# Performance work log

Hardware: AMD Instinct MI355X
Metric: run time of the kernel (lower is better)

Reference implementation:

```python
import jax, jax.numpy as jnp
import numpy as np

N = 50000        # nodes
E = 800000       # edges
D_IN = 512       # input_shape
PROJ = 256       # proj_dim
H = 4            # num_heads
C = 32           # hidden_channels
HC = H * C
NUM_LABELS = 10
SLOPE = 0.2      # GATv2 LeakyReLU negative slope


def _glorot(key, shape):
    fan_in = shape[-1]
    return jax.random.normal(key, shape, jnp.float32) / jnp.sqrt(jnp.float32(fan_in))


def setup_inputs() -> dict:
    key = jax.random.key(0)
    ks = jax.random.split(key, 16)
    inp = {}
    inp["x"] = jax.random.normal(ks[0], (N, D_IN), jnp.float32)
    inp["edge_index"] = jax.random.randint(ks[1], (2, E), 0, N, dtype=jnp.int64)
    # projection Linear
    inp["W_proj"] = _glorot(ks[2], (PROJ, D_IN)); inp["b_proj"] = jnp.zeros((PROJ,), jnp.float32)
    # GATv2 layer 1: lin_l, lin_r, att, bias
    inp["Wl1"] = _glorot(ks[3], (HC, PROJ)); inp["bl1"] = jnp.zeros((HC,), jnp.float32)
    inp["Wr1"] = _glorot(ks[4], (HC, PROJ)); inp["br1"] = jnp.zeros((HC,), jnp.float32)
    inp["att1"] = _glorot(ks[5], (H, C)); inp["bias1"] = jnp.zeros((HC,), jnp.float32)
    # GATv2 layer 2
    inp["Wl2"] = _glorot(ks[6], (HC, HC)); inp["bl2"] = jnp.zeros((HC,), jnp.float32)
    inp["Wr2"] = _glorot(ks[7], (HC, HC)); inp["br2"] = jnp.zeros((HC,), jnp.float32)
    inp["att2"] = _glorot(ks[8], (H, C)); inp["bias2"] = jnp.zeros((HC,), jnp.float32)
    # head MLP
    inp["W1"] = _glorot(ks[9], (C, HC)); inp["b1"] = jnp.zeros((C,), jnp.float32)
    inp["W2"] = _glorot(ks[10], (NUM_LABELS, C)); inp["b2"] = jnp.zeros((NUM_LABELS,), jnp.float32)
    return inp


def _gatv2(x, src, dst, Wl, bl, Wr, br, att, bias):
    # x: [N, F_in]; src/dst: [E]. PyG GATv2Conv, concat=True, no self-loops, eval (no dropout).
    xl = (x @ Wl.T + bl).reshape(N, H, C)   # source transform
    xr = (x @ Wr.T + br).reshape(N, H, C)   # target transform
    e = jax.nn.leaky_relu(xl[src] + xr[dst], negative_slope=SLOPE)  # [E,H,C]
    logit = jnp.einsum('ehc,hc->eh', e, att)                        # [E,H]
    # segment softmax over incoming edges of each destination node
    m = jax.ops.segment_max(logit, dst, num_segments=N)             # [N,H]
    m = jnp.where(jnp.isfinite(m), m, jnp.float32(0))               # empty segments -> 0
    p = jnp.exp(logit - m[dst])                                     # [E,H]
    s = jax.ops.segment_sum(p, dst, num_segments=N)                 # [N,H]
    alpha = p / (s[dst] + jnp.float32(1e-16))                       # [E,H]
    out = jax.ops.segment_sum(xl[src] * alpha[:, :, None], dst, num_segments=N)  # [N,H,C]
    return out.reshape(N, HC) + bias


def reference(x, edge_index, W_proj, b_proj, Wl1, bl1, Wr1, br1, att1, bias1,
              Wl2, bl2, Wr2, br2, att2, bias2, W1, b1, W2, b2):
    src, dst = edge_index[0], edge_index[1]
    h = jax.nn.elu(x @ W_proj.T + b_proj)
    h = jax.nn.elu(_gatv2(h, src, dst, Wl1, bl1, Wr1, br1, att1, bias1))
    h = jax.nn.elu(_gatv2(h, src, dst, Wl2, bl2, Wr2, br2, att2, bias2))
    h = jax.nn.elu(h @ W1.T + b1)
    return h @ W2.T + b2
```

## Files before the change

### kernel.cpp

```cpp
#include <hip/hip_runtime.h>
#include <cstdint>
#include <cstddef>

constexpr int NN = 50000;
constexpr int NE = 800000;

typedef _Float16 half8 __attribute__((ext_vector_type(8)));
typedef _Float16 half4v __attribute__((ext_vector_type(4)));
typedef _Float16 half2v __attribute__((ext_vector_type(2)));
typedef float f32x16 __attribute__((ext_vector_type(16)));
typedef unsigned short ushort_t;

__device__ inline ushort_t f2h(float f) {
  _Float16 h = (_Float16)f;
  return __builtin_bit_cast(ushort_t, h);
}

#if __has_builtin(__builtin_amdgcn_fdot2)
__device__ inline float fdot2(half2v a, half2v b, float c) {
  return __builtin_amdgcn_fdot2(a, b, c, false);
}
#else
__device__ inline float fdot2(half2v a, half2v b, float c) {
  return c + (float)a[0] * (float)b[0] + (float)a[1] * (float)b[1];
}
#endif

__global__ void k_wconv(const float* __restrict__ W, ushort_t* __restrict__ Bh,
                        int M, int K, int total) {
  int idx = blockIdx.x * 256 + threadIdx.x;
  if (idx >= total) return;
  int j = idx & 7;
  int l = (idx >> 3) & 63;
  int blk = idx >> 9;
  int nKB = K >> 4;
  int cb = blk / nKB, kb = blk - cb * nKB;
  int col = cb * 32 + (l & 31);
  int k = kb * 16 + ((l >> 5) & 1) * 8 + j;
  float v = (col < M) ? W[(size_t)col * K + k] : 0.f;
  Bh[idx] = f2h(v);
}

__global__ __launch_bounds__(512) void gemm_proj_l1(const float* __restrict__ x,
    const ushort_t* __restrict__ WpF, const ushort_t* __restrict__ WB1,
    const float* __restrict__ bp, const float* __restrict__ bl1,
    const float* __restrict__ br1, ushort_t* __restrict__ xlh,
    ushort_t* __restrict__ xrh, int N)
{
  constexpr int NKK = 4;
  constexpr int nKB1 = 32;
  constexpr int nK1 = 8;
  __shared__ ushort_t Ah[2][2 * NKK * 512];
  __shared__ ushort_t H0[16384];
  const int t = threadIdx.x;
  const int lane = t & 63;
  const int wid = t >> 6;
  const int wr = wid >> 2;
  const int wc = wid & 3;
  const int row0 = blockIdx.x * 64;
  const int cb0 = wc * 2;

  const int s_r = t >> 4, s_k = (t & 15) * 4;
  const int sb0 = (s_k >> 4) * 512 + (s_r + 32 * ((s_k >> 3) & 1)) * 8 + (s_k & 7);
  const int sb1 = sb0 + NKK * 512;
  const bool ok0 = (row0 + s_r) < N;
  const bool ok1 = (row0 + s_r + 32) < N;
  const float* ap0 = x + (size_t)(row0 + s_r) * 512 + s_k;
  const float* ap1 = x + (size_t)(row0 + s_r + 32) * 512 + s_k;

  f32x16 acc0 = {}, acc1 = {};
  float4 f0 = make_float4(0, 0, 0, 0), f1 = make_float4(0, 0, 0, 0);

  auto aload = [&](int ks) {
    f0 = make_float4(0, 0, 0, 0);
    f1 = make_float4(0, 0, 0, 0);
    if (ok0) f0 = *(const float4*)(ap0 + (size_t)ks * 64);
    if (ok1) f1 = *(const float4*)(ap1 + (size_t)ks * 64);
  };
  auto cvt4 = [](float4 f) {
    half4v h;
    h[0] = (_Float16)f.x; h[1] = (_Float16)f.y;
    h[2] = (_Float16)f.z; h[3] = (_Float16)f.w;
    return h;
  };
  auto stage_write = [&](int buf) {
    *(half4v*)&Ah[buf][sb0] = cvt4(f0);
    *(half4v*)&Ah[buf][sb1] = cvt4(f1);
  };

  aload(0);
  stage_write(0);
  __syncthreads();

  for (int ks = 0; ks < nK1; ++ks) {
    const int cur = ks & 1;
    const int nxt = cur ^ 1;
    const bool have_next = (ks + 1 < nK1);
    if (have_next) aload(ks + 1);

    #pragma unroll
    for (int kk = 0; kk < NKK; ++kk) {
      const int kbg = ks * NKK + kk;
      half8 ah = *(const half8*)&Ah[cur][(wr * NKK + kk) * 512 + lane * 8];
      const size_t bo0 = ((size_t)(cb0 * nKB1 + kbg) * 64 + lane) * 8;
      half8 bh0 = *(const half8*)(WpF + bo0);
      acc0 = __builtin_amdgcn_mfma_f32_32x32x16_f16(ah, bh0, acc0, 0, 0, 0);
      const size_t bo1 = ((size_t)((cb0 + 1) * nKB1 + kbg) * 64 + lane) * 8;
      half8 bh1 = *(const half8*)(WpF + bo1);
      acc1 = __builtin_amdgcn_mfma_f32_32x32x16_f16(ah, bh1, acc1, 0, 0, 0);
    }

    if (have_next) stage_write(nxt);
    __syncthreads();
  }

  {
    int col = cb0 * 32 + (lane & 31);
    float bv = bp[col];
    #pragma unroll
    for (int r = 0; r < 16; ++r) {
      int row = wr * 32 + (r & 3) + 8 * (r >> 2) + 4 * (lane >> 5);
      float v = acc0[r] + bv;
      v = v > 0.f ? v : (__expf(v) - 1.f);
      H0[((row >> 5) * 16 + (col >> 4)) * 512 +
         ((row & 31) + 32 * ((col >> 3) & 1)) * 8 + (col & 7)] = f2h(v);
    }
    int col1 = col + 32;
    float bv1 = bp[col1];
    #pragma unroll
    for (int r = 0; r < 16; ++r) {
      int row = wr * 32 + (r & 3) + 8 * (r >> 2) + 4 * (lane >> 5);
      float v = acc1[r] + bv1;
      v = v > 0.f ? v : (__expf(v) - 1.f);
      H0[((row >> 5) * 16 + (col1 >> 4)) * 512 +
         ((row & 31) + 32 * ((col1 >> 3) & 1)) * 8 + (col1 & 7)] = f2h(v);
    }
  }
  __syncthreads();

  f32x16 acc2a = {}, acc2b = {};
  #pragma unroll
  for (int kk = 0; kk < 16; ++kk) {
    half8 ah = *(const half8*)&H0[(wr * 16 + kk) * 512 + lane * 8];
    const size_t bo0 = ((size_t)(cb0 * 16 + kk) * 64 + lane) * 8;
    half8 bh0 = *(const half8*)(WB1 + bo0);
    acc2a = __builtin_amdgcn_mfma_f32_32x32x16_f16(ah, bh0, acc2a, 0, 0, 0);
    const size_t bo1 = ((size_t)((cb0 + 1) * 16 + kk) * 64 + lane) * 8;
    half8 bh1 = *(const half8*)(WB1 + bo1);
    acc2b = __builtin_amdgcn_mfma_f32_32x32x16_f16(ah, bh1, acc2b, 0, 0, 0);
  }

  auto epi2 = [&](const f32x16& acc, int cb) {
    int cc = cb * 32 + (lane & 31);
    float bv = (cc < 128) ? bl1[cc] : br1[cc - 128];
    #pragma unroll
    for (int r = 0; r < 16; ++r) {
      int rr = row0 + wr * 32 + (r & 3) + 8 * (r >> 2) + 4 * (lane >> 5);
      if (rr < N) {
        float v = acc[r] + bv;
        if (cc < 128) xlh[(size_t)rr * 128 + cc] = f2h(v);
        else          xrh[(size_t)rr * 128 + (cc - 128)] = f2h(v);
      }
    }
  };
  epi2(acc2a, cb0);
  epi2(acc2b, cb0 + 1);
}

__global__ __launch_bounds__(512) void gemm_mlp(const ushort_t* __restrict__ h2,
    const ushort_t* __restrict__ W1F, const ushort_t* __restrict__ W2F,
    const float* __restrict__ b1, const float* __restrict__ b2,
    float* __restrict__ out, int N)
{
  constexpr int NKK = 4;
  __shared__ ushort_t Ah[2][2 * NKK * 512];
  __shared__ ushort_t H3[2048];
  const int t = threadIdx.x;
  const int lane = t & 63;
  const int wid = t >> 6;
  const int wr = wid >> 2;
  const int wc = wid & 3;
  const int row0 = blockIdx.x * 64;

  const int s_r = t >> 3, s_k = (t & 7) * 8;
  const int sb0 = ((s_r >> 5) * NKK + (s_k >> 4)) * 512 +
                  ((s_r & 31) + 32 * ((s_k >> 3) & 1)) * 8;
  const bool ok0 = (row0 + s_r) < N;
  const ushort_t* aph = h2 + (size_t)(row0 + s_r) * 128 + s_k;

  f32x16 acc = {};
  half8 h8 = {};

  auto aload = [&](int ks) {
    half8 z = {};
    h8 = ok0 ? *(const half8*)(aph + (size_t)ks * 64) : z;
  };

  aload(0);
  *(half8*)&Ah[0][sb0] = h8;
  __syncthreads();

  for (int ks = 0; ks < 2; ++ks) {
    const int cur = ks & 1;
    const bool have_next = (ks == 0);
    if (have_next) aload(1);

    if (wc == 0) {
      #pragma unroll
      for (int kk = 0; kk < NKK; ++kk) {
        const int kbg = ks * NKK + kk;
        half8 ah = *(const half8*)&Ah[cur][(wr * NKK + kk) * 512 + lane * 8];
        half8 bh = *(const half8*)(W1F + ((size_t)kbg * 64 + lane) * 8);
        acc = __builtin_amdgcn_mfma_f32_32x32x16_f16(ah, bh, acc, 0, 0, 0);
      }
    }

    if (have_next) *(half8*)&Ah[cur ^ 1][sb0] = h8;
    __syncthreads();
  }

  if (wc == 0) {
    int cc = lane & 31;
    float bv = b1[cc];
    #pragma unroll
    for (int r = 0; r < 16; ++r) {
      int row = wr * 32 + (r & 3) + 8 * (r >> 2) + 4 * (lane >> 5);
      float v = acc[r] + bv;
      v = v > 0.f ? v : (__expf(v) - 1.f);
      H3[((row >> 5) * 2 + (cc >> 4)) * 512 +
         ((row & 31) + 32 * ((cc >> 3) & 1)) * 8 + (cc & 7)] = f2h(v);
    }
  }
  __syncthreads();

  if (wc == 0) {
    f32x16 acc2 = {};
    #pragma unroll
    for (int kk = 0; kk < 2; ++kk) {
      half8 ah = *(const half8*)&H3[(wr * 2 + kk) * 512 + lane * 8];
      half8 bh = *(const half8*)(W2F + ((size_t)kk * 64 + lane) * 8);
      acc2 = __builtin_amdgcn_mfma_f32_32x32x16_f16(ah, bh, acc2, 0, 0, 0);
    }
    int cc = lane & 31;
    if (cc < 10) {
      float bv = b2[cc];
      #pragma unroll
      for (int r = 0; r < 16; ++r) {
        int rr = row0 + wr * 32 + (r & 3) + 8 * (r >> 2) + 4 * (lane >> 5);
        if (rr < N) out[(size_t)rr * 10 + cc] = acc2[r] + bv;
      }
    }
  }
}

template<int ACT, int OUTMODE, int BKT, int AFP16, int NCB>
__global__ __launch_bounds__(512) void gemm_mfma(const void* __restrict__ Av,
    const ushort_t* __restrict__ Bh,
    const float* __restrict__ bias, const float* __restrict__ bias2,
    float* __restrict__ C, ushort_t* __restrict__ C16a,
    ushort_t* __restrict__ C16b, int N, int M, int K)
{
  constexpr int NKK = BKT / 16;
  __shared__ ushort_t Ah[2][2 * NKK * 512];
  const int t = threadIdx.x;
  const int lane = t & 63;
  const int wid = t >> 6;
  const int wr = wid >> 2;
  const int wc = wid & 3;
  const int row0 = blockIdx.x * 64;
  const int col0 = blockIdx.y * (128 * NCB);
  const int nKB = K >> 4;
  const int nK = K / BKT;
  const int cb0 = (col0 >> 5) + wc * NCB;

  int s_r, s_k, sb0, sb1 = 0;
  bool ok0 = false, ok1 = false;
  if constexpr (!AFP16) {
    s_r = t >> 4; s_k = (t & 15) * 4;
    sb0 = (s_k >> 4) * 512 + (s_r + 32 * ((s_k >> 3) & 1)) * 8 + (s_k & 7);
    sb1 = sb0 + NKK * 512;
    ok0 = (row0 + s_r) < N;
    ok1 = (row0 + s_r + 32) < N;
  } else if constexpr (BKT == 64) {
    s_r = t >> 3; s_k = (t & 7) * 8;
    sb0 = ((s_r >> 5) * NKK + (s_k >> 4)) * 512 +
          ((s_r & 31) + 32 * ((s_k >> 3) & 1)) * 8;
    ok0 = (row0 + s_r) < N;
  } else {
    s_r = t >> 3; s_k = (t & 7) * 4;
    sb0 = ((s_r >> 5) * NKK + (s_k >> 4)) * 512 +
          ((s_r & 31) + 32 * ((s_k >> 3) & 1)) * 8 + (s_k & 7);
    ok0 = (row0 + s_r) < N;
  }
  const float*    ap0 = (const float*)Av + (size_t)(row0 + s_r) * K + s_k;
  const float*    ap1 = (const float*)Av + (size_t)(row0 + s_r + 32) * K + s_k;
  const ushort_t* aph = (const ushort_t*)Av + (size_t)(row0 + s_r) * K + s_k;

  f32x16 acc0 = {}, acc1 = {};
  float4 f0 = make_float4(0, 0, 0, 0), f1 = make_float4(0, 0, 0, 0);
  half8 h8 = {};
  half4v h4 = {};

  auto aload = [&](int ks) {
    if constexpr (!AFP16) {
      f0 = make_float4(0, 0, 0, 0);
      f1 = make_float4(0, 0, 0, 0);
      if (ok0) f0 = *(const float4*)(ap0 + (size_t)ks * BKT);
      if (ok1) f1 = *(const float4*)(ap1 + (size_t)ks * BKT);
    } else if constexpr (BKT == 64) {
      half8 z = {};
      h8 = ok0 ? *(const half8*)(aph + (size_t)ks * BKT) : z;
    } else {
      half4v z = {};
      h4 = ok0 ? *(const half4v*)(aph + (size_t)ks * BKT) : z;
    }
  };
  auto cvt4 = [](float4 f) {
    half4v h;
    h[0] = (_Float16)f.x; h[1] = (_Float16)f.y;
    h[2] = (_Float16)f.z; h[3] = (_Float16)f.w;
    return h;
  };
  auto stage_write = [&](int buf) {
    if constexpr (!AFP16) {
      *(half4v*)&Ah[buf][sb0] = cvt4(f0);
      *(half4v*)&Ah[buf][sb1] = cvt4(f1);
    } else if constexpr (BKT == 64) {
      *(half8*)&Ah[buf][sb0] = h8;
    } else {
      *(half4v*)&Ah[buf][sb0] = h4;
    }
  };

  aload(0);
  stage_write(0);
  __syncthreads();

  for (int ks = 0; ks < nK; ++ks) {
    const int cur = ks & 1;
    const int nxt = cur ^ 1;
    const bool have_next = (ks + 1 < nK);
    if (have_next) aload(ks + 1);

    #pragma unroll
    for (int kk = 0; kk < NKK; ++kk) {
      const int kbg = ks * NKK + kk;
      half8 ah = *(const half8*)&Ah[cur][(wr * NKK + kk) * 512 + lane * 8];
      const size_t bo0 = ((size_t)(cb0 * nKB + kbg) * 64 + lane) * 8;
      half8 bh0 = *(const half8*)(Bh + bo0);
      acc0 = __builtin_amdgcn_mfma_f32_32x32x16_f16(ah, bh0, acc0, 0, 0, 0);
      if constexpr (NCB == 2) {
        const size_t bo1 = ((size_t)((cb0 + 1) * nKB + kbg) * 64 + lane) * 8;
        half8 bh1 = *(const half8*)(Bh + bo1);
        acc1 = __builtin_amdgcn_mfma_f32_32x32x16_f16(ah, bh1, acc1, 0, 0, 0);
      }
    }

    if (have_next) stage_write(nxt);
    __syncthreads();
  }

  auto epi = [&](const f32x16& acc, int cb) {
    int cc = cb * 32 + (lane & 31);
    float bv;
    if constexpr (OUTMODE == 3) bv = (cc < 128) ? bias[cc] : bias2[cc - 128];
    else                        bv = (cc < M) ? bias[cc] : 0.f;
    #pragma unroll
    for (int r = 0; r < 16; ++r) {
      int rr = row0 + wr * 32 + (r & 3) + 8 * (r >> 2) + 4 * (lane >> 5);
      if (rr < N && cc < M) {
        float v = acc[r] + bv;
        if (ACT) v = v > 0.f ? v : (__expf(v) - 1.f);
        if constexpr (OUTMODE == 0)      C[(size_t)rr * M + cc] = v;
        else if constexpr (OUTMODE == 1) C16a[(size_t)rr * M + cc] = f2h(v);
        else {
          if (cc < 128) C16a[(size_t)rr * 128 + cc] = f2h(v);
          else          C16b[(size_t)rr * 128 + (cc - 128)] = f2h(v);
        }
      }
    }
  };
  epi(acc0, cb0);
  if constexpr (NCB == 2) epi(acc1, cb0 + 1);
}

__global__ void k_degrank(const int* __restrict__ ei, int* __restrict__ deg,
                          int* __restrict__ rank) {
  int e = blockIdx.x * 256 + threadIdx.x;
  if (e >= NE) return;
  int d = ei[NE + e];
  rank[e] = atomicAdd(&deg[d], 1);
}

__global__ __launch_bounds__(256) void k_scan1(const int* __restrict__ deg,
    int* __restrict__ rowstart, int* __restrict__ blocksum) {
  __shared__ int sm[256];
  int b = blockIdx.x, t = threadIdx.x;
  int i = b * 256 + t;
  int v = (i < NN) ? deg[i] : 0;
  sm[t] = v;
  __syncthreads();
  #pragma unroll
  for (int off = 1; off < 256; off <<= 1) {
    int u = (t >= off) ? sm[t - off] : 0;
    __syncthreads();
    sm[t] += u;
    __syncthreads();
  }
  if (i < NN) rowstart[i + 1] = sm[t];
  if (t == 255) blocksum[b] = sm[255];
}

__global__ __launch_bounds__(256) void k_scan2(int* __restrict__ blocksum, int nb) {
  __shared__ int sm[256];
  int t = threadIdx.x;
  int v = (t < nb) ? blocksum[t] : 0;
  sm[t] = v;
  __syncthreads();
  #pragma unroll
  for (int off = 1; off < 256; off <<= 1) {
    int u = (t >= off) ? sm[t - off] : 0;
    __syncthreads();
    sm[t] += u;
    __syncthreads();
  }
  if (t < nb) blocksum[t] = (t == 0) ? 0 : sm[t - 1];
}

__global__ __launch_bounds__(256) void k_scan3(int* __restrict__ rowstart,
    const int* __restrict__ blocksum) {
  int b = blockIdx.x, t = threadIdx.x;
  int i = b * 256 + t;
  if (i == 0) rowstart[0] = 0;
  if (i < NN) rowstart[i + 1] += blocksum[b];
}

__global__ void k_scatter(const int* __restrict__ ei, const int* __restrict__ rowstart,
                          const int* __restrict__ rank, int* __restrict__ srcp) {
  int e = blockIdx.x * 256 + threadIdx.x;
  if (e >= NE) return;
  int d = ei[NE + e];
  srcp[rowstart[d] + rank[e]] = ei[e];
}

__global__ __launch_bounds__(256) void k_gat(const ushort_t* __restrict__ xl,
    const ushort_t* __restrict__ xr, const int* __restrict__ srcp,
    const int* __restrict__ rowstart, const float* __restrict__ att,
    const float* __restrict__ bias, ushort_t* __restrict__ out)
{
  const int g = threadIdx.x >> 5;
  const int c = threadIdx.x & 31;
  const int n = blockIdx.x * 8 + g;
  const int r0 = rowstart[n], r1 = rowstart[n + 1];
  half4v xrh = *(const half4v*)(xr + (size_t)n * 128 + 4 * c);
  const half2v xr01 = {xrh[0], xrh[1]};
  const half2v xr23 = {xrh[2], xrh[3]};
  const float4 atv = *(const float4*)(att + 4 * c);
  const half2v at01 = {(_Float16)atv.x, (_Float16)atv.y};
  const half2v at23 = {(_Float16)atv.z, (_Float16)atv.w};
  const half2v k02 = {(_Float16)0.2f, (_Float16)0.2f};

  float m = -1e30f, ssum = 0.f;
  float a0 = 0.f, a1 = 0.f, a2 = 0.f, a3 = 0.f;

  auto lg = [&](int s, float4& xs) -> float {
    half4v hv = *(const half4v*)(xl + (size_t)s * 128 + 4 * c);
    xs.x = (float)hv[0]; xs.y = (float)hv[1];
    xs.z = (float)hv[2]; xs.w = (float)hv[3];
    half2v u01 = half2v{hv[0], hv[1]} + xr01;
    half2v u23 = half2v{hv[2], hv[3]} + xr23;
    u01 = __builtin_elementwise_max(u01, u01 * k02);
    u23 = __builtin_elementwise_max(u23, u23 * k02);
    float l = fdot2(u01, at01, fdot2(u23, at23, 0.f));
    l += __shfl_xor(l, 1);
    l += __shfl_xor(l, 2);
    l += __shfl_xor(l, 4);
    return l;
  };

  const int je = r1 - 1;
  for (int j = r0; j < r1; j += 8) {
    int s0 = srcp[j];
    int s1 = srcp[min(j + 1, je)], s2 = srcp[min(j + 2, je)];
    int s3 = srcp[min(j + 3, je)], s4 = srcp[min(j + 4, je)];
    int s5 = srcp[min(j + 5, je)], s6 = srcp[min(j + 6, je)];
    int s7 = srcp[min(j + 7, je)];
    float4 x0, x1, x2, x3, x4, x5, x6, x7;
    float l0 = lg(s0, x0), l1 = lg(s1, x1), l2 = lg(s2, x2), l3 = lg(s3, x3);
    float l4 = lg(s4, x4), l5 = lg(s5, x5), l6 = lg(s6, x6), l7 = lg(s7, x7);
    l1 = (j + 1 < r1) ? l1 : -1e30f;
    l2 = (j + 2 < r1) ? l2 : -1e30f;
    l3 = (j + 3 < r1) ? l3 : -1e30f;
    l4 = (j + 4 < r1) ? l4 : -1e30f;
    l5 = (j + 5 < r1) ? l5 : -1e30f;
    l6 = (j + 6 < r1) ? l6 : -1e30f;
    l7 = (j + 7 < r1) ? l7 : -1e30f;
    float mloc = fmaxf(fmaxf(fmaxf(l0, l1), fmaxf(l2, l3)),
                       fmaxf(fmaxf(l4, l5), fmaxf(l6, l7)));
    float mn = fmaxf(m, mloc);
    float sc = __expf(m - mn);
    float p0 = __expf(l0 - mn), p1 = __expf(l1 - mn);
    float p2 = __expf(l2 - mn), p3 = __expf(l3 - mn);
    float p4 = __expf(l4 - mn), p5 = __expf(l5 - mn);
    float p6 = __expf(l6 - mn), p7 = __expf(l7 - mn);
    ssum = ssum * sc + (((p0 + p1) + (p2 + p3)) + ((p4 + p5) + (p6 + p7)));
    a0 = a0 * sc + (((p0 * x0.x + p1 * x1.x) + (p2 * x2.x + p3 * x3.x)) +
                    ((p4 * x4.x + p5 * x5.x) + (p6 * x6.x + p7 * x7.x)));
    a1 = a1 * sc + (((p0 * x0.y + p1 * x1.y) + (p2 * x2.y + p3 * x3.y)) +
                    ((p4 * x4.y + p5 * x5.y) + (p6 * x6.y + p7 * x7.y)));
    a2 = a2 * sc + (((p0 * x0.z + p1 * x1.z) + (p2 * x2.z + p3 * x3.z)) +
                    ((p4 * x4.z + p5 * x5.z) + (p6 * x6.z + p7 * x7.z)));
    a3 = a3 * sc + (((p0 * x0.w + p1 * x1.w) + (p2 * x2.w + p3 * x3.w)) +
                    ((p4 * x4.w + p5 * x5.w) + (p6 * x6.w + p7 * x7.w)));
    m = mn;
  }

  const float4 bv = *(const float4*)(bias + 4 * c);
  float rinv = 1.f / (ssum + 1e-16f);
  float o0 = a0 * rinv + bv.x;
  float o1 = a1 * rinv + bv.y;
  float o2 = a2 * rinv + bv.z;
  float o3 = a3 * rinv + bv.w;
  o0 = o0 > 0.f ? o0 : (__expf(o0) - 1.f);
  o1 = o1 > 0.f ? o1 : (__expf(o1) - 1.f);
  o2 = o2 > 0.f ? o2 : (__expf(o2) - 1.f);
  o3 = o3 > 0.f ? o3 : (__expf(o3) - 1.f);
  half4v ov;
  ov[0] = (_Float16)o0; ov[1] = (_Float16)o1;
  ov[2] = (_Float16)o2; ov[3] = (_Float16)o3;
  *(half4v*)(out + (size_t)n * 128 + 4 * c) = ov;
}

__global__ void k_report_ws(float* out, int out_size, float wsz) {
  int i = blockIdx.x * 256 + threadIdx.x;
  if (i < out_size) out[i] = (i == 0) ? wsz : 0.f;
}

extern "C" void kernel_launch(void* const* d_in, const int* in_sizes, int n_in,
                              void* d_out, int out_size, void* d_ws, size_t ws_size,
                              hipStream_t stream)
{
  const float* x    = (const float*)d_in[0];
  const int*   ei   = (const int*)d_in[1];
  const float* Wp   = (const float*)d_in[2];  const float* bp    = (const float*)d_in[3];
  const float* Wl1  = (const float*)d_in[4];  const float* bl1   = (const float*)d_in[5];
  const float* Wr1  = (const float*)d_in[6];  const float* br1   = (const float*)d_in[7];
  const float* att1 = (const float*)d_in[8];  const float* bias1 = (const float*)d_in[9];
  const float* Wl2  = (const float*)d_in[10]; const float* bl2   = (const float*)d_in[11];
  const float* Wr2  = (const float*)d_in[12]; const float* br2   = (const float*)d_in[13];
  const float* att2 = (const float*)d_in[14]; const float* bias2 = (const float*)d_in[15];
  const float* W1   = (const float*)d_in[16]; const float* b1    = (const float*)d_in[17];
  const float* W2   = (const float*)d_in[18]; const float* b2    = (const float*)d_in[19];
  float* out = (float*)d_out;

  constexpr size_t NEED = 122300000;
  if (ws_size < NEED) {
    k_report_ws<<<(out_size + 255) / 256, 256, 0, stream>>>(out, out_size, (float)ws_size);
    return;
  }
  char* ws = (char*)d_ws;
  ushort_t* h1h   = (ushort_t*)(ws + 0);
  ushort_t* h2h   = (ushort_t*)(ws + 25600000);
  ushort_t* xlh   = (ushort_t*)(ws + 51200000);
  ushort_t* xrh   = (ushort_t*)(ws + 76800000);
  ushort_t* wb    = (ushort_t*)(ws + 108800000);
  int*      srcp  = (int*)(ws + 115200000);
  int*      rank  = (int*)(ws + 118400000);
  int*      deg   = (int*)(ws + 121600000);
  int*      rowst = (int*)(ws + 122000000);
  int*      bsum  = (int*)(ws + 122250000);

  ushort_t* Wph  = wb;
  ushort_t* WB1h = wb + 131072;
  ushort_t* WB2h = wb + 196608;
  ushort_t* W1h  = wb + 229376;
  ushort_t* W2h  = wb + 233472;

  hipMemsetAsync(deg, 0, NN * sizeof(int), stream);

  k_wconv<<<(131072+255)/256, 256, 0, stream>>>(Wp,  Wph,          256, 512, 131072);
  k_wconv<<<(32768+255)/256,  256, 0, stream>>>(Wl1, WB1h,         128, 256, 32768);
  k_wconv<<<(32768+255)/256,  256, 0, stream>>>(Wr1, WB1h + 32768, 128, 256, 32768);
  k_wconv<<<(16384+255)/256,  256, 0, stream>>>(Wl2, WB2h,         128, 128, 16384);
  k_wconv<<<(16384+255)/256,  256, 0, stream>>>(Wr2, WB2h + 16384, 128, 128, 16384);
  k_wconv<<<(4096+255)/256,   256, 0, stream>>>(W1,  W1h,          32,  128, 4096);
  k_wconv<<<(1024+255)/256,   256, 0, stream>>>(W2,  W2h,          10,  32,  1024);

  constexpr int NB = (NN + 255) / 256;
  k_degrank<<<(NE+255)/256, 256, 0, stream>>>(ei, deg, rank);
  k_scan1  <<<NB, 256, 0, stream>>>(deg, rowst, bsum);
  k_scan2  <<<1, 256, 0, stream>>>(bsum, NB);
  k_scan3  <<<NB, 256, 0, stream>>>(rowst, bsum);
  k_scatter<<<(NE+255)/256, 256, 0, stream>>>(ei, rowst, rank, srcp);

  constexpr int GX = (NN + 63) / 64;

  gemm_proj_l1<<<GX, 512, 0, stream>>>(x, Wph, WB1h, bp, bl1, br1, xlh, xrh, NN);
  k_gat<<<NN/8, 256, 0, stream>>>(xlh, xrh, srcp, rowst, att1, bias1, h1h);

  gemm_mfma<0,3,64,1,2><<<dim3(GX, 1), 512, 0, stream>>>(
      h1h, WB2h, bl2, br2, nullptr, xlh, xrh, NN, 256, 128);
  k_gat<<<NN/8, 256, 0, stream>>>(xlh, xrh, srcp, rowst, att2, bias2, h2h);

  gemm_mlp<<<GX, 512, 0, stream>>>(h2h, W1h, W2h, b1, b2, out, NN);
}
```

Measured before the change: 240.7 us.

## Pre-convert x to fp16 and stage GEMM A tiles via direct global-to-LDS loads

Adds a separate kernel that converts the fp32 input x to fp16, so the fused projection GEMM can load A tiles with global_load_lds (direct DMA into shared memory) instead of loading to registers, converting, and storing to LDS. The same direct-to-LDS staging is applied to a new specialized layer-2 GEMM, which replaces the generic templated kernel, and to the MLP GEMM. Boundary rows are clamped rather than zero-filled, and the workspace is relaid out. The extra conversion pass reads x and writes an fp16 copy, adding memory traffic that has to be repaid by the simpler GEMM load path.

```diff
diff --git a/kernel.cpp b/kernel.cpp
--- a/kernel.cpp
+++ b/kernel.cpp
@@ -25,6 +25,26 @@
   return c + (float)a[0] * (float)b[0] + (float)a[1] * (float)b[1];
 }
 #endif
+
+__device__ __forceinline__ void gload_lds16(const void* g, void* l) {
+  __builtin_amdgcn_global_load_lds(
+      (const __attribute__((address_space(1))) void*)g,
+      (__attribute__((address_space(3))) void*)l, 16, 0, 0);
+}
+
+__global__ __launch_bounds__(256) void k_cvt(const float* __restrict__ x,
+                                             ushort_t* __restrict__ xh) {
+  int i = blockIdx.x * 256 + threadIdx.x;
+  if (i >= NN * 512 / 8) return;
+  const float4* p = (const float4*)(x + (size_t)i * 8);
+  float4 a = p[0], b = p[1];
+  half8 h;
+  h[0] = (_Float16)a.x; h[1] = (_Float16)a.y;
+  h[2] = (_Float16)a.z; h[3] = (_Float16)a.w;
+  h[4] = (_Float16)b.x; h[5] = (_Float16)b.y;
+  h[6] = (_Float16)b.z; h[7] = (_Float16)b.w;
+  *(half8*)(xh + (size_t)i * 8) = h;
+}
 
 __global__ void k_wconv(const float* __restrict__ W, ushort_t* __restrict__ Bh,
                         int M, int K, int total) {
@@ -41,7 +61,7 @@
   Bh[idx] = f2h(v);
 }
 
-__global__ __launch_bounds__(512) void gemm_proj_l1(const float* __restrict__ x,
+__global__ __launch_bounds__(512) void gemm_proj_l1(const ushort_t* __restrict__ xh,
     const ushort_t* __restrict__ WpF, const ushort_t* __restrict__ WB1,
     const float* __restrict__ bp, const float* __restrict__ bl1,
     const float* __restrict__ br1, ushort_t* __restrict__ xlh,
@@ -50,7 +70,7 @@
   constexpr int NKK = 4;
   constexpr int nKB1 = 32;
   constexpr int nK1 = 8;
-  __shared__ ushort_t Ah[2][2 * NKK * 512];
+  __shared__ ushort_t Ah[2][8 * 512];
   __shared__ ushort_t H0[16384];
   const int t = threadIdx.x;
   const int lane = t & 63;
@@ -60,43 +80,20 @@
   const int row0 = blockIdx.x * 64;
   const int cb0 = wc * 2;
 
-  const int s_r = t >> 4, s_k = (t & 15) * 4;
-  const int sb0 = (s_k >> 4) * 512 + (s_r + 32 * ((s_k >> 3) & 1)) * 8 + (s_k & 7);
-  const int sb1 = sb0 + NKK * 512;
-  const bool ok0 = (row0 + s_r) < N;
-  const bool ok1 = (row0 + s_r + 32) < N;
-  const float* ap0 = x + (size_t)(row0 + s_r) * 512 + s_k;
-  const float* ap1 = x + (size_t)(row0 + s_r + 32) * 512 + s_k;
+  const int swt = wid >> 2, skb = wid & 3;
+  const int grow = min(row0 + swt * 32 + (lane & 31), N - 1);
+  const ushort_t* gA = xh + (size_t)grow * 512 + skb * 16 + (lane >> 5) * 8;
+  ushort_t* ld0 = &Ah[0][wid * 512];
+  ushort_t* ld1 = &Ah[1][wid * 512];
 
   f32x16 acc0 = {}, acc1 = {};
-  float4 f0 = make_float4(0, 0, 0, 0), f1 = make_float4(0, 0, 0, 0);
-
-  auto aload = [&](int ks) {
-    f0 = make_float4(0, 0, 0, 0);
-    f1 = make_float4(0, 0, 0, 0);
-    if (ok0) f0 = *(const float4*)(ap0 + (size_t)ks * 64);
-    if (ok1) f1 = *(const float4*)(ap1 + (size_t)ks * 64);
-  };
-  auto cvt4 = [](float4 f) {
-    half4v h;
-    h[0] = (_Float16)f.x; h[1] = (_Float16)f.y;
-    h[2] = (_Float16)f.z; h[3] = (_Float16)f.w;
-    return h;
-  };
-  auto stage_write = [&](int buf) {
-    *(half4v*)&Ah[buf][sb0] = cvt4(f0);
-    *(half4v*)&Ah[buf][sb1] = cvt4(f1);
-  };
-
-  aload(0);
-  stage_write(0);
+
+  gload_lds16(gA, ld0);
   __syncthreads();
 
   for (int ks = 0; ks < nK1; ++ks) {
     const int cur = ks & 1;
-    const int nxt = cur ^ 1;
-    const bool have_next = (ks + 1 < nK1);
-    if (have_next) aload(ks + 1);
+    if (ks + 1 < nK1) gload_lds16(gA + (size_t)(ks + 1) * 64, cur ? ld0 : ld1);
 
     #pragma unroll
     for (int kk = 0; kk < NKK; ++kk) {
@@ -109,8 +106,6 @@
       half8 bh1 = *(const half8*)(WpF + bo1);
       acc1 = __builtin_amdgcn_mfma_f32_32x32x16_f16(ah, bh1, acc1, 0, 0, 0);
     }
-
-    if (have_next) stage_write(nxt);
     __syncthreads();
   }
 
@@ -167,13 +162,76 @@
   epi2(acc2b, cb0 + 1);
 }
 
+__global__ __launch_bounds__(512) void gemm_l2(const ushort_t* __restrict__ h1,
+    const ushort_t* __restrict__ WB2, const float* __restrict__ bl2,
+    const float* __restrict__ br2, ushort_t* __restrict__ xlh,
+    ushort_t* __restrict__ xrh, int N)
+{
+  constexpr int NKK = 4;
+  constexpr int nKB = 8;
+  constexpr int nK = 2;
+  __shared__ ushort_t Ah[2][8 * 512];
+  const int t = threadIdx.x;
+  const int lane = t & 63;
+  const int wid = t >> 6;
+  const int wr = wid >> 2;
+  const int wc = wid & 3;
+  const int row0 = blockIdx.x * 64;
+  const int cb0 = wc * 2;
+
+  const int swt = wid >> 2, skb = wid & 3;
+  const int grow = min(row0 + swt * 32 + (lane & 31), N - 1);
+  const ushort_t* gA = h1 + (size_t)grow * 128 + skb * 16 + (lane >> 5) * 8;
+  ushort_t* ld0 = &Ah[0][wid * 512];
+  ushort_t* ld1 = &Ah[1][wid * 512];
+
+  f32x16 acc0 = {}, acc1 = {};
+
+  gload_lds16(gA, ld0);
+  __syncthreads();
+
+  for (int ks = 0; ks < nK; ++ks) {
+    const int cur = ks & 1;
+    if (ks + 1 < nK) gload_lds16(gA + (size_t)(ks + 1) * 64, cur ? ld0 : ld1);
+
+    #pragma unroll
+    for (int kk = 0; kk < NKK; ++kk) {
+      const int kbg = ks * NKK + kk;
+      half8 ah = *(const half8*)&Ah[cur][(wr * NKK + kk) * 512 + lane * 8];
+      const size_t bo0 = ((size_t)(cb0 * nKB + kbg) * 64 + lane) * 8;
+      half8 bh0 = *(const half8*)(WB2 + bo0);
+      acc0 = __builtin_amdgcn_mfma_f32_32x32x16_f16(ah, bh0, acc0, 0, 0, 0);
+      const size_t bo1 = ((size_t)((cb0 + 1) * nKB + kbg) * 64 + lane) * 8;
+      half8 bh1 = *(const half8*)(WB2 + bo1);
+      acc1 = __builtin_amdgcn_mfma_f32_32x32x16_f16(ah, bh1, acc1, 0, 0, 0);
+    }
+    __syncthreads();
+  }
+
+  auto epi = [&](const f32x16& acc, int cb) {
+    int cc = cb * 32 + (lane & 31);
+    float bv = (cc < 128) ? bl2[cc] : br2[cc - 128];
+    #pragma unroll
+    for (int r = 0; r < 16; ++r) {
+      int rr = row0 + wr * 32 + (r & 3) + 8 * (r >> 2) + 4 * (lane >> 5);
+      if (rr < N) {
+        float v = acc[r] + bv;
+        if (cc < 128) xlh[(size_t)rr * 128 + cc] = f2h(v);
+        else          xrh[(size_t)rr * 128 + (cc - 128)] = f2h(v);
+      }
+    }
+  };
+  epi(acc0, cb0);
+  epi(acc1, cb0 + 1);
+}
+
 __global__ __launch_bounds__(512) void gemm_mlp(const ushort_t* __restrict__ h2,
     const ushort_t* __restrict__ W1F, const ushort_t* __restrict__ W2F,
     const float* __restrict__ b1, const float* __restrict__ b2,
     float* __restrict__ out, int N)
 {
   constexpr int NKK = 4;
-  __shared__ ushort_t Ah[2][2 * NKK * 512];
+  __shared__ ushort_t Ah[2][8 * 512];
   __shared__ ushort_t H3[2048];
   const int t = threadIdx.x;
   const int lane = t & 63;
@@ -182,28 +240,20 @@
   const int wc = wid & 3;
   const int row0 = blockIdx.x * 64;
 
-  const int s_r = t >> 3, s_k = (t & 7) * 8;
-  const int sb0 = ((s_r >> 5) * NKK + (s_k >> 4)) * 512 +
-                  ((s_r & 31) + 32 * ((s_k >> 3) & 1)) * 8;
-  const bool ok0 = (row0 + s_r) < N;
-  const ushort_t* aph = h2 + (size_t)(row0 + s_r) * 128 + s_k;
+  const int swt = wid >> 2, skb = wid & 3;
+  const int grow = min(row0 + swt * 32 + (lane & 31), N - 1);
+  const ushort_t* gA = h2 + (size_t)grow * 128 + skb * 16 + (lane >> 5) * 8;
+  ushort_t* ld0 = &Ah[0][wid * 512];
+  ushort_t* ld1 = &Ah[1][wid * 512];
 
   f32x16 acc = {};
-  half8 h8 = {};
-
-  auto aload = [&](int ks) {
-    half8 z = {};
-    h8 = ok0 ? *(const half8*)(aph + (size_t)ks * 64) : z;
-  };
-
-  aload(0);
-  *(half8*)&Ah[0][sb0] = h8;
+
+  gload_lds16(gA, ld0);
   __syncthreads();
 
   for (int ks = 0; ks < 2; ++ks) {
     const int cur = ks & 1;
-    const bool have_next = (ks == 0);
-    if (have_next) aload(1);
+    if (ks + 1 < 2) gload_lds16(gA + (size_t)(ks + 1) * 64, cur ? ld0 : ld1);
 
     if (wc == 0) {
       #pragma unroll
@@ -214,8 +264,6 @@
         acc = __builtin_amdgcn_mfma_f32_32x32x16_f16(ah, bh, acc, 0, 0, 0);
       }
     }
-
-    if (have_next) *(half8*)&Ah[cur ^ 1][sb0] = h8;
     __syncthreads();
   }
 
@@ -251,137 +299,6 @@
       }
     }
   }
-}
-
-template<int ACT, int OUTMODE, int BKT, int AFP16, int NCB>
-__global__ __launch_bounds__(512) void gemm_mfma(const void* __restrict__ Av,
-    const ushort_t* __restrict__ Bh,
-    const float* __restrict__ bias, const float* __restrict__ bias2,
-    float* __restrict__ C, ushort_t* __restrict__ C16a,
-    ushort_t* __restrict__ C16b, int N, int M, int K)
-{
-  constexpr int NKK = BKT / 16;
-  __shared__ ushort_t Ah[2][2 * NKK * 512];
-  const int t = threadIdx.x;
-  const int lane = t & 63;
-  const int wid = t >> 6;
-  const int wr = wid >> 2;
-  const int wc = wid & 3;
-  const int row0 = blockIdx.x * 64;
-  const int col0 = blockIdx.y * (128 * NCB);
-  const int nKB = K >> 4;
-  const int nK = K / BKT;
-  const int cb0 = (col0 >> 5) + wc * NCB;
-
-  int s_r, s_k, sb0, sb1 = 0;
-  bool ok0 = false, ok1 = false;
-  if constexpr (!AFP16) {
-    s_r = t >> 4; s_k = (t & 15) * 4;
-    sb0 = (s_k >> 4) * 512 + (s_r + 32 * ((s_k >> 3) & 1)) * 8 + (s_k & 7);
-    sb1 = sb0 + NKK * 512;
-    ok0 = (row0 + s_r) < N;
-    ok1 = (row0 + s_r + 32) < N;
-  } else if constexpr (BKT == 64) {
-    s_r = t >> 3; s_k = (t & 7) * 8;
-    sb0 = ((s_r >> 5) * NKK + (s_k >> 4)) * 512 +
-          ((s_r & 31) + 32 * ((s_k >> 3) & 1)) * 8;
-    ok0 = (row0 + s_r) < N;
-  } else {
-    s_r = t >> 3; s_k = (t & 7) * 4;
-    sb0 = ((s_r >> 5) * NKK + (s_k >> 4)) * 512 +
-          ((s_r & 31) + 32 * ((s_k >> 3) & 1)) * 8 + (s_k & 7);
-    ok0 = (row0 + s_r) < N;
-  }
-  const float*    ap0 = (const float*)Av + (size_t)(row0 + s_r) * K + s_k;
-  const float*    ap1 = (const float*)Av + (size_t)(row0 + s_r + 32) * K + s_k;
-  const ushort_t* aph = (const ushort_t*)Av + (size_t)(row0 + s_r) * K + s_k;
-
-  f32x16 acc0 = {}, acc1 = {};
-  float4 f0 = make_float4(0, 0, 0, 0), f1 = make_float4(0, 0, 0, 0);
-  half8 h8 = {};
-  half4v h4 = {};
-
-  auto aload = [&](int ks) {
-    if constexpr (!AFP16) {
-      f0 = make_float4(0, 0, 0, 0);
-      f1 = make_float4(0, 0, 0, 0);
-      if (ok0) f0 = *(const float4*)(ap0 + (size_t)ks * BKT);
-      if (ok1) f1 = *(const float4*)(ap1 + (size_t)ks * BKT);
-    } else if constexpr (BKT == 64) {
-      half8 z = {};
-      h8 = ok0 ? *(const half8*)(aph + (size_t)ks * BKT) : z;
-    } else {
-      half4v z = {};
-      h4 = ok0 ? *(const half4v*)(aph + (size_t)ks * BKT) : z;
-    }
-  };
-  auto cvt4 = [](float4 f) {
-    half4v h;
-    h[0] = (_Float16)f.x; h[1] = (_Float16)f.y;
-    h[2] = (_Float16)f.z; h[3] = (_Float16)f.w;
-    return h;
-  };
-  auto stage_write = [&](int buf) {
-    if constexpr (!AFP16) {
-      *(half4v*)&Ah[buf][sb0] = cvt4(f0);
-      *(half4v*)&Ah[buf][sb1] = cvt4(f1);
-    } else if constexpr (BKT == 64) {
-      *(half8*)&Ah[buf][sb0] = h8;
-    } else {
-      *(half4v*)&Ah[buf][sb0] = h4;
-    }
-  };
-
-  aload(0);
-  stage_write(0);
-  __syncthreads();
-
-  for (int ks = 0; ks < nK; ++ks) {
-    const int cur = ks & 1;
-    const int nxt = cur ^ 1;
-    const bool have_next = (ks + 1 < nK);
-    if (have_next) aload(ks + 1);
-
-    #pragma unroll
-    for (int kk = 0; kk < NKK; ++kk) {
-      const int kbg = ks * NKK + kk;
-      half8 ah = *(const half8*)&Ah[cur][(wr * NKK + kk) * 512 + lane * 8];
-      const size_t bo0 = ((size_t)(cb0 * nKB + kbg) * 64 + lane) * 8;
-      half8 bh0 = *(const half8*)(Bh + bo0);
-      acc0 = __builtin_amdgcn_mfma_f32_32x32x16_f16(ah, bh0, acc0, 0, 0, 0);
-      if constexpr (NCB == 2) {
-        const size_t bo1 = ((size_t)((cb0 + 1) * nKB + kbg) * 64 + lane) * 8;
-        half8 bh1 = *(const half8*)(Bh + bo1);
-        acc1 = __builtin_amdgcn_mfma_f32_32x32x16_f16(ah, bh1, acc1, 0, 0, 0);
-      }
-    }
-
-    if (have_next) stage_write(nxt);
-    __syncthreads();
-  }
-
-  auto epi = [&](const f32x16& acc, int cb) {
-    int cc = cb * 32 + (lane & 31);
-    float bv;
-    if constexpr (OUTMODE == 3) bv = (cc < 128) ? bias[cc] : bias2[cc - 128];
-    else                        bv = (cc < M) ? bias[cc] : 0.f;
-    #pragma unroll
-    for (int r = 0; r < 16; ++r) {
-      int rr = row0 + wr * 32 + (r & 3) + 8 * (r >> 2) + 4 * (lane >> 5);
-      if (rr < N && cc < M) {
-        float v = acc[r] + bv;
-        if (ACT) v = v > 0.f ? v : (__expf(v) - 1.f);
-        if constexpr (OUTMODE == 0)      C[(size_t)rr * M + cc] = v;
-        else if constexpr (OUTMODE == 1) C16a[(size_t)rr * M + cc] = f2h(v);
-        else {
-          if (cc < 128) C16a[(size_t)rr * 128 + cc] = f2h(v);
-          else          C16b[(size_t)rr * 128 + (cc - 128)] = f2h(v);
-        }
-      }
-    }
-  };
-  epi(acc0, cb0);
-  if constexpr (NCB == 2) epi(acc1, cb0 + 1);
 }
 
 __global__ void k_degrank(const int* __restrict__ ei, int* __restrict__ deg,
@@ -559,16 +476,17 @@
     return;
   }
   char* ws = (char*)d_ws;
-  ushort_t* h1h   = (ushort_t*)(ws + 0);
-  ushort_t* h2h   = (ushort_t*)(ws + 25600000);
+  ushort_t* xh    = (ushort_t*)(ws + 0);
   ushort_t* xlh   = (ushort_t*)(ws + 51200000);
-  ushort_t* xrh   = (ushort_t*)(ws + 76800000);
-  ushort_t* wb    = (ushort_t*)(ws + 108800000);
-  int*      srcp  = (int*)(ws + 115200000);
-  int*      rank  = (int*)(ws + 118400000);
-  int*      deg   = (int*)(ws + 121600000);
-  int*      rowst = (int*)(ws + 122000000);
-  int*      bsum  = (int*)(ws + 122250000);
+  ushort_t* xrh   = (ushort_t*)(ws + 64000000);
+  ushort_t* h1h   = (ushort_t*)(ws + 76800000);
+  ushort_t* h2h   = (ushort_t*)(ws + 89600000);
+  ushort_t* wb    = (ushort_t*)(ws + 102400000);
+  int*      srcp  = (int*)(ws + 103400000);
+  int*      rank  = (int*)(ws + 106600000);
+  int*      deg   = (int*)(ws + 109800000);
+  int*      rowst = (int*)(ws + 110000000);
+  int*      bsum  = (int*)(ws + 110250000);
 
   ushort_t* Wph  = wb;
   ushort_t* WB1h = wb + 131072;
@@ -577,6 +495,8 @@
   ushort_t* W2h  = wb + 233472;
 
   hipMemsetAsync(deg, 0, NN * sizeof(int), stream);
+
+  k_cvt<<<(NN * 512 / 8 + 255) / 256, 256, 0, stream>>>(x, xh);
 
   k_wconv<<<(131072+255)/256, 256, 0, stream>>>(Wp,  Wph,          256, 512, 131072);
   k_wconv<<<(32768+255)/256,  256, 0, stream>>>(Wl1, WB1h,         128, 256, 32768);
@@ -595,11 +515,10 @@
 
   constexpr int GX = (NN + 63) / 64;
 
-  gemm_proj_l1<<<GX, 512, 0, stream>>>(x, Wph, WB1h, bp, bl1, br1, xlh, xrh, NN);
+  gemm_proj_l1<<<GX, 512, 0, stream>>>(xh, Wph, WB1h, bp, bl1, br1, xlh, xrh, NN);
   k_gat<<<NN/8, 256, 0, stream>>>(xlh, xrh, srcp, rowst, att1, bias1, h1h);
 
-  gemm_mfma<0,3,64,1,2><<<dim3(GX, 1), 512, 0, stream>>>(
-      h1h, WB2h, bl2, br2, nullptr, xlh, xrh, NN, 256, 128);
+  gemm_l2<<<GX, 512, 0, stream>>>(h1h, WB2h, bl2, br2, xlh, xrh, NN);
   k_gat<<<NN/8, 256, 0, stream>>>(xlh, xrh, srcp, rowst, att2, bias2, h2h);
 
   gemm_mlp<<<GX, 512, 0, stream>>>(h2h, W1h, W2h, b1, b2, out, NN);
```

Measured after the change: 251.4 us. 4.4% more time.
